# Kernel optimization log

Hardware: AMD Instinct MI355X
Metric: run time of the kernel (lower is better)

Reference implementation:

```python
import jax, jax.numpy as jnp
import numpy as np

NUM_USERS = 100000
NUM_ITEMS = 50000
N_NODES = NUM_USERS + NUM_ITEMS
EMB = 64          # emb_dim == layers[0]
NNZ = 2_400_000   # ~16 avg degree normalized-Laplacian nonzeros
BATCH = 16384


def spmm(rows, cols, vals, x, n):
    # sparse (COO) Laplacian @ dense features: out[r] += v * x[c]
    return jax.ops.segment_sum(vals[:, None] * x[cols], rows, num_segments=n)


def setup_inputs() -> dict:
    key = jax.random.key(0)
    ks = jax.random.split(key, 20)
    userIdx = jax.random.randint(ks[0], (BATCH,), 0, NUM_USERS)
    itemIdx = jax.random.randint(ks[1], (BATCH,), 0, NUM_ITEMS)
    lap_rows = jax.random.randint(ks[2], (NNZ,), 0, N_NODES, dtype=jnp.int32)
    lap_cols = jax.random.randint(ks[3], (NNZ,), 0, N_NODES, dtype=jnp.int32)
    # normalized Laplacian values ~ 1/sqrt(deg_i*deg_j), small positive
    lap_vals = jax.random.uniform(ks[4], (NNZ,), dtype=jnp.float32) * 0.05
    uEmb = jax.random.normal(ks[5], (NUM_USERS, EMB), dtype=jnp.float32) * 0.1
    iEmb = jax.random.normal(ks[6], (NUM_ITEMS, EMB), dtype=jnp.float32) * 0.1
    s = 1.0 / np.sqrt(EMB)
    gW0 = jax.random.normal(ks[7], (EMB, EMB), dtype=jnp.float32) * s
    gb0 = jnp.zeros((EMB,), jnp.float32)
    gW1 = jax.random.normal(ks[8], (EMB, EMB), dtype=jnp.float32) * s
    gb1 = jnp.zeros((EMB,), jnp.float32)
    D_CAT = EMB * 3 * 2  # 384
    W1 = jax.random.normal(ks[9], (D_CAT, 64), dtype=jnp.float32) / np.sqrt(D_CAT)
    b1 = jnp.zeros((64,), jnp.float32)
    W2 = jax.random.normal(ks[10], (64, 32), dtype=jnp.float32) / 8.0
    b2 = jnp.zeros((32,), jnp.float32)
    W3 = jax.random.normal(ks[11], (32, 1), dtype=jnp.float32) / np.sqrt(32.0)
    b3 = jnp.zeros((1,), jnp.float32)
    return {"userIdx": userIdx, "itemIdx": itemIdx,
            "lap_rows": lap_rows, "lap_cols": lap_cols, "lap_vals": lap_vals,
            "uEmb": uEmb, "iEmb": iEmb,
            "gW0": gW0, "gb0": gb0, "gW1": gW1, "gb1": gb1,
            "W1": W1, "b1": b1, "W2": W2, "b2": b2, "W3": W3, "b3": b3}


def reference(userIdx, itemIdx, lap_rows, lap_cols, lap_vals,
              uEmb, iEmb, gW0, gb0, gW1, gb1, W1, b1, W2, b2, W3, b3):
    features = jnp.concatenate([uEmb, iEmb], axis=0)  # [N, EMB]
    final = features
    for W, b in ((gW0, gb0), (gW1, gb1)):
        # (Laplacian + selfLoop I) @ features, then linear + ReLU
        h = spmm(lap_rows, lap_cols, lap_vals, features, N_NODES) + features
        features = jax.nn.relu(h @ W + b)
        final = jnp.concatenate([final, features], axis=1)
    u = final[userIdx]                     # [B, 192]
    it = final[itemIdx + NUM_USERS]        # [B, 192]
    e = jnp.concatenate([u, it], axis=1)   # [B, 384]
    e = jax.nn.relu(e @ W1 + b1)
    e = e @ W2 + b2
    e = e @ W3 + b3
    return e.ravel()
```

## Files before the change

kernel.cpp:

```cpp
#include <hip/hip_runtime.h>
#include <hip/hip_bf16.h>

#define NUM_USERS 100000
#define NUM_ITEMS 50000
#define N_NODES   150000
#define EMB       64
#define NNZ       2400000
#define BATCH     16384
#define D_CAT     384
#define BSHIFT    8
#define NBUCK     ((N_NODES + 255) >> 8)
#define EPB       8192

__device__ __forceinline__ unsigned short f2bf(float f) {
    unsigned u = __float_as_uint(f);
    unsigned r = u + 0x7fffu + ((u >> 16) & 1u);
    return (unsigned short)(r >> 16);
}
__device__ __forceinline__ float bflo(unsigned u) { return __uint_as_float(u << 16); }
__device__ __forceinline__ float bfhi(unsigned u) { return __uint_as_float(u & 0xffff0000u); }

__global__ __launch_bounds__(1024) void bucket_hist(const int* __restrict__ rows,
                                                    int* __restrict__ bcnt, int nnz) {
    __shared__ int h[NBUCK];
    int tid = threadIdx.x;
    for (int i = tid; i < NBUCK; i += 1024) h[i] = 0;
    __syncthreads();
    for (int i = blockIdx.x * 1024 + tid; i < nnz; i += gridDim.x * 1024)
        atomicAdd(&h[rows[i] >> BSHIFT], 1);
    __syncthreads();
    for (int i = tid; i < NBUCK; i += 1024) {
        int c = h[i];
        if (c) atomicAdd(&bcnt[i], c);
    }
}

__global__ __launch_bounds__(1024) void bucket_scan(const int* __restrict__ bcnt,
                                                    int* __restrict__ boffs,
                                                    int* __restrict__ gtails, int nnz) {
    __shared__ int s[1024];
    int t = threadIdx.x;
    int x = (t < NBUCK) ? bcnt[t] : 0;
    s[t] = x;
    __syncthreads();
#pragma unroll
    for (int off = 1; off < 1024; off <<= 1) {
        int v = (t >= off) ? s[t - off] : 0;
        __syncthreads();
        s[t] += v;
        __syncthreads();
    }
    if (t < NBUCK) {
        int e = s[t] - x;
        boffs[t] = e;
        gtails[t] = e;
    }
    if (t == 0) boffs[NBUCK] = nnz;
}

__global__ __launch_bounds__(1024) void coarse_multisplit(const int* __restrict__ rows,
                                                          const int* __restrict__ cols,
                                                          const float* __restrict__ vals,
                                                          int* __restrict__ gtails,
                                                          int2* __restrict__ pv, int nnz) {
    __shared__ int hcnt[NBUCK];
    int tid = threadIdx.x;
    int e0 = blockIdx.x * EPB;
    int e1 = e0 + EPB < nnz ? e0 + EPB : nnz;

    for (int i = tid; i < NBUCK; i += 1024) hcnt[i] = 0;
    __syncthreads();
    for (int i = e0 + tid; i < e1; i += 1024)
        atomicAdd(&hcnt[rows[i] >> BSHIFT], 1);
    __syncthreads();
    for (int i = tid; i < NBUCK; i += 1024) {
        int c = hcnt[i];
        if (c) hcnt[i] = atomicAdd(&gtails[i], c);
    }
    __syncthreads();
    for (int i = e0 + tid; i < e1; i += 1024) {
        int r = rows[i];
        int pos = atomicAdd(&hcnt[r >> BSHIFT], 1);
        pv[pos] = make_int2(((r & 255) << 18) | cols[i], __float_as_int(vals[i]));
    }
}

__global__ __launch_bounds__(1024) void fine_scatter(const int* __restrict__ boffs,
                                                     const int2* __restrict__ pv,
                                                     int2* __restrict__ packed,
                                                     int* __restrict__ row_ptr, int nnz) {
    __shared__ int rcnt[256];
    __shared__ int loff[256];
    int b = blockIdx.x;
    int tid = threadIdx.x;
    int lo = boffs[b], hi = boffs[b + 1];
    int r0 = b << BSHIFT;
    int nr = N_NODES - r0; if (nr > 256) nr = 256;

    if (tid < 256) rcnt[tid] = 0;
    __syncthreads();
    for (int i = lo + tid; i < hi; i += 1024)
        atomicAdd(&rcnt[pv[i].x >> 18], 1);
    __syncthreads();
    if (tid < 256) loff[tid] = rcnt[tid];
    __syncthreads();
#pragma unroll
    for (int off = 1; off < 256; off <<= 1) {
        int v = (tid < 256 && tid >= off) ? loff[tid - off] : 0;
        __syncthreads();
        if (tid < 256) loff[tid] += v;
        __syncthreads();
    }
    if (tid < 256) {
        int e = lo + loff[tid] - rcnt[tid];
        loff[tid] = e;
        if (tid < nr) row_ptr[r0 + tid] = e;
    }
    if (b == 0 && tid == 0) row_ptr[N_NODES] = nnz;
    __syncthreads();
    for (int i = lo + tid; i < hi; i += 1024) {
        int2 e = pv[i];
        int rl = e.x >> 18;
        int pos = atomicAdd(&loff[rl], 1);
        packed[pos] = make_int2(e.x & 0x3FFFF, e.y);
    }
}

__global__ __launch_bounds__(256) void gemm_table_f32(const float* __restrict__ uE,
                                                      const float* __restrict__ iE,
                                                      const float* __restrict__ W,
                                                      unsigned short* __restrict__ Zh,
                                                      int n_rows) {
    __shared__ float Wl[64 * 64];
    __shared__ float Xf[64 * 64];
    int tid = threadIdx.x;
    int lane = tid & 63;
    int wave = tid >> 6;
    int r0 = blockIdx.x * 64;
    int last = n_rows - 1;

    for (int i = tid; i < 64 * 64; i += 256) Wl[i] = W[i];
    for (int i = tid; i < 64 * 16; i += 256) {
        int row = i >> 4, q = i & 15;
        int r = r0 + row; r = r > last ? last : r;
        const float4* src = (r < NUM_USERS)
            ? (const float4*)(uE + (size_t)r * 64)
            : (const float4*)(iE + (size_t)(r - NUM_USERS) * 64);
        ((float4*)Xf)[i] = src[q];
    }
    __syncthreads();

    int rbase = wave * 16;
    float acc[16];
#pragma unroll
    for (int i = 0; i < 16; ++i) acc[i] = 0.f;

#pragma unroll 1
    for (int kc = 0; kc < 16; ++kc) {
        float w0 = Wl[(kc * 4 + 0) * 64 + lane];
        float w1 = Wl[(kc * 4 + 1) * 64 + lane];
        float w2 = Wl[(kc * 4 + 2) * 64 + lane];
        float w3 = Wl[(kc * 4 + 3) * 64 + lane];
#pragma unroll
        for (int i = 0; i < 16; ++i) {
            float4 q = ((const float4*)Xf)[(rbase + i) * 16 + kc];
            acc[i] = fmaf(q.x, w0, acc[i]);
            acc[i] = fmaf(q.y, w1, acc[i]);
            acc[i] = fmaf(q.z, w2, acc[i]);
            acc[i] = fmaf(q.w, w3, acc[i]);
        }
    }
#pragma unroll
    for (int i = 0; i < 16; ++i) {
        int r = r0 + rbase + i;
        if (r < n_rows) Zh[(size_t)r * 64 + lane] = f2bf(acc[i]);
    }
}

__global__ __launch_bounds__(256) void gemm_table_bf16(const unsigned* __restrict__ Xh,
                                                       const float* __restrict__ W,
                                                       unsigned short* __restrict__ Zh,
                                                       int n_rows) {
    __shared__ float Wl[64 * 64];
    __shared__ uint4 Xl4[64 * 8];
    int tid = threadIdx.x;
    int lane = tid & 63;
    int wave = tid >> 6;
    int r0 = blockIdx.x * 64;
    int nr = n_rows - r0; if (nr > 64) nr = 64;

    for (int i = tid; i < 64 * 64; i += 256) Wl[i] = W[i];
    const uint4* Xg4 = (const uint4*)(Xh + (size_t)r0 * 32);
    for (int i = tid; i < nr * 8; i += 256) Xl4[i] = Xg4[i];
    __syncthreads();

    const unsigned* Xl = (const unsigned*)Xl4;
    int rbase = wave * 16;
    float acc[16];
#pragma unroll
    for (int i = 0; i < 16; ++i) acc[i] = 0.f;

#pragma unroll 1
    for (int kc = 0; kc < 8; ++kc) {
        float w0 = Wl[(kc * 8 + 0) * 64 + lane];
        float w1 = Wl[(kc * 8 + 1) * 64 + lane];
        float w2 = Wl[(kc * 8 + 2) * 64 + lane];
        float w3 = Wl[(kc * 8 + 3) * 64 + lane];
        float w4 = Wl[(kc * 8 + 4) * 64 + lane];
        float w5 = Wl[(kc * 8 + 5) * 64 + lane];
        float w6 = Wl[(kc * 8 + 6) * 64 + lane];
        float w7 = Wl[(kc * 8 + 7) * 64 + lane];
#pragma unroll
        for (int i = 0; i < 16; ++i) {
            uint4 q = *(const uint4*)&Xl[(rbase + i) * 32 + kc * 4];
            acc[i] = fmaf(bflo(q.x), w0, acc[i]);
            acc[i] = fmaf(bfhi(q.x), w1, acc[i]);
            acc[i] = fmaf(bflo(q.y), w2, acc[i]);
            acc[i] = fmaf(bfhi(q.y), w3, acc[i]);
            acc[i] = fmaf(bflo(q.z), w4, acc[i]);
            acc[i] = fmaf(bfhi(q.z), w5, acc[i]);
            acc[i] = fmaf(bflo(q.w), w6, acc[i]);
            acc[i] = fmaf(bfhi(q.w), w7, acc[i]);
        }
    }
#pragma unroll
    for (int i = 0; i < 16; ++i) {
        int r = r0 + rbase + i;
        if (r < n_rows) Zh[(size_t)r * 64 + lane] = f2bf(acc[i]);
    }
}

__global__ __launch_bounds__(256) void spmm_bias_relu(const int* __restrict__ row_ptr,
                                                      const int2* __restrict__ packed,
                                                      const uint2* __restrict__ zh2,
                                                      const float* __restrict__ bias,
                                                      uint2* __restrict__ outh2,
                                                      int n_rows) {
    int tid = threadIdx.x;
    int lane = tid & 63;
    int wave = tid >> 6;
    int q = lane >> 4;
    int k = lane & 15;
    int r = blockIdx.x * 4 + wave;
    if (r >= n_rows) return;

    uint2 su = zh2[(size_t)r * 16 + k];
    float4 acc;
    acc.x = q ? 0.f : bflo(su.x);
    acc.y = q ? 0.f : bfhi(su.x);
    acc.z = q ? 0.f : bflo(su.y);
    acc.w = q ? 0.f : bfhi(su.y);

    int e = row_ptr[r] + q;
    int end = row_ptr[r + 1];
    for (; e + 13 < end; e += 16) {
        int2 p0 = packed[e + 0];
        int2 p1 = packed[e + 4];
        int2 p2 = packed[e + 8];
        int2 p3 = packed[e + 12];
        uint2 z0 = zh2[(size_t)p0.x * 16 + k];
        uint2 z1 = zh2[(size_t)p1.x * 16 + k];
        uint2 z2 = zh2[(size_t)p2.x * 16 + k];
        uint2 z3 = zh2[(size_t)p3.x * 16 + k];
        float v0 = __int_as_float(p0.y), v1 = __int_as_float(p1.y);
        float v2 = __int_as_float(p2.y), v3 = __int_as_float(p3.y);
        acc.x = fmaf(v0, bflo(z0.x), acc.x); acc.y = fmaf(v0, bfhi(z0.x), acc.y);
        acc.z = fmaf(v0, bflo(z0.y), acc.z); acc.w = fmaf(v0, bfhi(z0.y), acc.w);
        acc.x = fmaf(v1, bflo(z1.x), acc.x); acc.y = fmaf(v1, bfhi(z1.x), acc.y);
        acc.z = fmaf(v1, bflo(z1.y), acc.z); acc.w = fmaf(v1, bfhi(z1.y), acc.w);
        acc.x = fmaf(v2, bflo(z2.x), acc.x); acc.y = fmaf(v2, bfhi(z2.x), acc.y);
        acc.z = fmaf(v2, bflo(z2.y), acc.z); acc.w = fmaf(v2, bfhi(z2.y), acc.w);
        acc.x = fmaf(v3, bflo(z3.x), acc.x); acc.y = fmaf(v3, bfhi(z3.x), acc.y);
        acc.z = fmaf(v3, bflo(z3.y), acc.z); acc.w = fmaf(v3, bfhi(z3.y), acc.w);
    }
    for (; e < end; e += 4) {
        int2 p = packed[e];
        uint2 z = zh2[(size_t)p.x * 16 + k];
        float v = __int_as_float(p.y);
        acc.x = fmaf(v, bflo(z.x), acc.x); acc.y = fmaf(v, bfhi(z.x), acc.y);
        acc.z = fmaf(v, bflo(z.y), acc.z); acc.w = fmaf(v, bfhi(z.y), acc.w);
    }

    acc.x += __shfl_xor(acc.x, 16, 64);
    acc.y += __shfl_xor(acc.y, 16, 64);
    acc.z += __shfl_xor(acc.z, 16, 64);
    acc.w += __shfl_xor(acc.w, 16, 64);
    acc.x += __shfl_xor(acc.x, 32, 64);
    acc.y += __shfl_xor(acc.y, 32, 64);
    acc.z += __shfl_xor(acc.z, 32, 64);
    acc.w += __shfl_xor(acc.w, 32, 64);
    if (q == 0) {
        float4 bv = ((const float4*)bias)[k];
        float a = fmaxf(acc.x + bv.x, 0.f);
        float b = fmaxf(acc.y + bv.y, 0.f);
        float c = fmaxf(acc.z + bv.z, 0.f);
        float d = fmaxf(acc.w + bv.w, 0.f);
        outh2[(size_t)r * 16 + k] = make_uint2(
            ((unsigned)f2bf(b) << 16) | (unsigned)f2bf(a),
            ((unsigned)f2bf(d) << 16) | (unsigned)f2bf(c));
    }
}

__global__ __launch_bounds__(384) void gather_e(const int* __restrict__ userIdx,
                                                const int* __restrict__ itemIdx,
                                                const float* __restrict__ uEmb,
                                                const float* __restrict__ iEmb,
                                                const unsigned short* __restrict__ feat1h,
                                                const unsigned short* __restrict__ feat2h,
                                                unsigned short* __restrict__ E) {
    int b = blockIdx.x;
    int j = threadIdx.x;
    int half = j >= 192;
    int jj = half ? (j - 192) : j;
    int seg = jj >> 6;
    int k = jj & 63;
    unsigned short v;
    if (half == 0) {
        int u = userIdx[b];
        if (seg == 0)      v = f2bf(uEmb[(size_t)u * 64 + k]);
        else if (seg == 1) v = feat1h[(size_t)u * 64 + k];
        else               v = feat2h[(size_t)u * 64 + k];
    } else {
        int it = itemIdx[b];
        if (seg == 0)      v = f2bf(iEmb[(size_t)it * 64 + k]);
        else if (seg == 1) v = feat1h[(size_t)(it + NUM_USERS) * 64 + k];
        else               v = feat2h[(size_t)(it + NUM_USERS) * 64 + k];
    }
    E[(size_t)b * D_CAT + j] = v;
}

__global__ __launch_bounds__(256) void gemm384_bf16_relu(const unsigned short* __restrict__ E,
                                                         const float* __restrict__ W,
                                                         const float* __restrict__ bia,
                                                         float* __restrict__ H1,
                                                         int n_rows) {
    __shared__ float Wl[128 * 64];
    __shared__ uint4 El[64 * 16];
    int tid = threadIdx.x;
    int lane = tid & 63;
    int wave = tid >> 6;
    int r0 = blockIdx.x * 64;
    int rbase = wave * 16;
    int last = n_rows - 1;

    float acc[16];
    float bv = bia[lane];
#pragma unroll
    for (int i = 0; i < 16; ++i) acc[i] = bv;

    for (int k0 = 0; k0 < D_CAT; k0 += 128) {
        if (k0) __syncthreads();
        for (int i = tid; i < 128 * 64; i += 256) Wl[i] = W[k0 * 64 + i];
        for (int i = tid; i < 64 * 16; i += 256) {
            int row = i >> 4, q = i & 15;
            int r = r0 + row; r = r > last ? last : r;
            El[i] = *(const uint4*)(E + (size_t)r * D_CAT + k0 + q * 8);
        }
        __syncthreads();
#pragma unroll 1
        for (int k = 0; k < 128; k += 8) {
            float w0 = Wl[(k + 0) * 64 + lane];
            float w1 = Wl[(k + 1) * 64 + lane];
            float w2 = Wl[(k + 2) * 64 + lane];
            float w3 = Wl[(k + 3) * 64 + lane];
            float w4 = Wl[(k + 4) * 64 + lane];
            float w5 = Wl[(k + 5) * 64 + lane];
            float w6 = Wl[(k + 6) * 64 + lane];
            float w7 = Wl[(k + 7) * 64 + lane];
#pragma unroll
            for (int i = 0; i < 16; ++i) {
                uint4 q = El[(rbase + i) * 16 + (k >> 3)];
                acc[i] = fmaf(bflo(q.x), w0, acc[i]);
                acc[i] = fmaf(bfhi(q.x), w1, acc[i]);
                acc[i] = fmaf(bflo(q.y), w2, acc[i]);
                acc[i] = fmaf(bfhi(q.y), w3, acc[i]);
                acc[i] = fmaf(bflo(q.z), w4, acc[i]);
                acc[i] = fmaf(bfhi(q.z), w5, acc[i]);
                acc[i] = fmaf(bflo(q.w), w6, acc[i]);
                acc[i] = fmaf(bfhi(q.w), w7, acc[i]);
            }
        }
    }
#pragma unroll
    for (int i = 0; i < 16; ++i) {
        int r = r0 + rbase + i;
        if (r < n_rows) H1[(size_t)r * 64 + lane] = fmaxf(acc[i], 0.f);
    }
}

__global__ __launch_bounds__(256) void mlp23(const float* __restrict__ H1,
                                             const float* __restrict__ W2,
                                             const float* __restrict__ b2,
                                             const float* __restrict__ W3,
                                             const float* __restrict__ b3,
                                             float* __restrict__ out) {
    __shared__ float Wl[64 * 32];
    __shared__ float w3l[32];
    __shared__ float b2l[32];
    int tid = threadIdx.x;
    for (int i = tid; i < 64 * 32; i += 256) Wl[i] = W2[i];
    if (tid < 32) { w3l[tid] = W3[tid]; b2l[tid] = b2[tid]; }
    __syncthreads();

    int lane = tid & 63;
    int wave = tid >> 6;
    int half = lane >> 5;
    int k = lane & 31;
    int gpair = blockIdx.x * 4 + wave;
    int npairs = gridDim.x * 4;
    float b3v = b3[0];
    for (int p = gpair; p * 2 < BATCH; p += npairs) {
        int r = p * 2 + half;
        float acc = b2l[k];
#pragma unroll
        for (int j = 0; j < 64; ++j)
            acc += H1[(size_t)r * 64 + j] * Wl[j * 32 + k];
        acc = acc * w3l[k];
#pragma unroll
        for (int off = 16; off; off >>= 1)
            acc += __shfl_xor(acc, off, 64);
        if (k == 0) out[r] = acc + b3v;
    }
}

extern "C" void kernel_launch(void* const* d_in, const int* in_sizes, int n_in,
                              void* d_out, int out_size, void* d_ws, size_t ws_size,
                              hipStream_t stream) {
    const int*   userIdx = (const int*)  d_in[0];
    const int*   itemIdx = (const int*)  d_in[1];
    const int*   lap_rows= (const int*)  d_in[2];
    const int*   lap_cols= (const int*)  d_in[3];
    const float* lap_vals= (const float*)d_in[4];
    const float* uEmb    = (const float*)d_in[5];
    const float* iEmb    = (const float*)d_in[6];
    const float* gW0     = (const float*)d_in[7];
    const float* gb0     = (const float*)d_in[8];
    const float* gW1     = (const float*)d_in[9];
    const float* gb1     = (const float*)d_in[10];
    const float* W1      = (const float*)d_in[11];
    const float* b1      = (const float*)d_in[12];
    const float* W2      = (const float*)d_in[13];
    const float* b2      = (const float*)d_in[14];
    const float* W3      = (const float*)d_in[15];
    const float* b3      = (const float*)d_in[16];
    float* out = (float*)d_out;

    const size_t NF = (size_t)N_NODES * EMB;
    char* w = (char*)d_ws;
    unsigned short* bufA = (unsigned short*)w;
    unsigned short* bufB = bufA + NF;
    char*  region3 = (char*)(bufB + NF);
    int2*  pv      = (int2*)region3;
    unsigned short* Zh = (unsigned short*)region3;
    unsigned short* E  = (unsigned short*)region3;
    float* H1 = (float*)(E + (size_t)BATCH * D_CAT);
    int2*  packed  = (int2*)(region3 + NF * sizeof(float));
    int*   row_ptr = (int*)(packed + NNZ);
    int*   boffs   = row_ptr + (N_NODES + 1);
    int*   gtails  = boffs + (NBUCK + 1);
    int*   bcnt    = gtails + NBUCK;

    const int ms_grid   = (NNZ + EPB - 1) / EPB;
    const int spmm_grid = (N_NODES + 3) / 4;
    const int gemm_grid = (N_NODES + 63) / 64;

    hipMemsetAsync(bcnt, 0, NBUCK * sizeof(int), stream);
    bucket_hist<<<128, 1024, 0, stream>>>(lap_rows, bcnt, NNZ);
    bucket_scan<<<1, 1024, 0, stream>>>(bcnt, boffs, gtails, NNZ);
    coarse_multisplit<<<ms_grid, 1024, 0, stream>>>(lap_rows, lap_cols, lap_vals,
                                                    gtails, pv, NNZ);
    fine_scatter<<<NBUCK, 1024, 0, stream>>>(boffs, pv, packed, row_ptr, NNZ);

    gemm_table_f32<<<gemm_grid, 256, 0, stream>>>(uEmb, iEmb, gW0, Zh, N_NODES);
    spmm_bias_relu<<<spmm_grid, 256, 0, stream>>>(row_ptr, packed, (const uint2*)Zh,
                                                  gb0, (uint2*)bufA, N_NODES);

    gemm_table_bf16<<<gemm_grid, 256, 0, stream>>>((const unsigned*)bufA, gW1, Zh, N_NODES);
    spmm_bias_relu<<<spmm_grid, 256, 0, stream>>>(row_ptr, packed, (const uint2*)Zh,
                                                  gb1, (uint2*)bufB, N_NODES);

    gather_e<<<BATCH, 384, 0, stream>>>(userIdx, itemIdx, uEmb, iEmb, bufA, bufB, E);

    gemm384_bf16_relu<<<(BATCH + 63) / 64, 256, 0, stream>>>(E, W1, b1, H1, BATCH);
    mlp23<<<512, 256, 0, stream>>>(H1, W2, b2, W3, b3, out);
}
```

Measured before the change: 517.4 us.

## Fuse embedding gather, first MLP layer and output head into one kernel

Replaces the separate gather_e, gemm384 and mlp23 kernels with a single kernel per 64-row batch tile. The tile gathers user/item rows straight into shared memory, runs the 384x64 layer, keeps the hidden activations in shared memory and finishes the 64->32->1 head locally. This removes two launches and the global round trips through the E and H1 buffers. In exchange it uses more shared memory per block (about 66 KB), which may lower occupancy, and the head stage runs on only 256 blocks.

New measurement: 492.5 us. 1.05x faster.

```diff
diff --git a/kernel.cpp b/kernel.cpp
--- a/kernel.cpp
+++ b/kernel.cpp
@@ -301,62 +301,70 @@
     }
 }
 
-__global__ __launch_bounds__(384) void gather_e(const int* __restrict__ userIdx,
-                                                const int* __restrict__ itemIdx,
-                                                const float* __restrict__ uEmb,
-                                                const float* __restrict__ iEmb,
-                                                const unsigned short* __restrict__ feat1h,
-                                                const unsigned short* __restrict__ feat2h,
-                                                unsigned short* __restrict__ E) {
-    int b = blockIdx.x;
-    int j = threadIdx.x;
-    int half = j >= 192;
-    int jj = half ? (j - 192) : j;
-    int seg = jj >> 6;
-    int k = jj & 63;
-    unsigned short v;
-    if (half == 0) {
-        int u = userIdx[b];
-        if (seg == 0)      v = f2bf(uEmb[(size_t)u * 64 + k]);
-        else if (seg == 1) v = feat1h[(size_t)u * 64 + k];
-        else               v = feat2h[(size_t)u * 64 + k];
-    } else {
-        int it = itemIdx[b];
-        if (seg == 0)      v = f2bf(iEmb[(size_t)it * 64 + k]);
-        else if (seg == 1) v = feat1h[(size_t)(it + NUM_USERS) * 64 + k];
-        else               v = feat2h[(size_t)(it + NUM_USERS) * 64 + k];
-    }
-    E[(size_t)b * D_CAT + j] = v;
-}
-
-__global__ __launch_bounds__(256) void gemm384_bf16_relu(const unsigned short* __restrict__ E,
-                                                         const float* __restrict__ W,
-                                                         const float* __restrict__ bia,
-                                                         float* __restrict__ H1,
-                                                         int n_rows) {
-    __shared__ float Wl[128 * 64];
-    __shared__ uint4 El[64 * 16];
+__global__ __launch_bounds__(256) void fused_mlp(
+        const int* __restrict__ userIdx, const int* __restrict__ itemIdx,
+        const float* __restrict__ uEmb, const float* __restrict__ iEmb,
+        const unsigned short* __restrict__ feat1h,
+        const unsigned short* __restrict__ feat2h,
+        const float* __restrict__ W1, const float* __restrict__ b1,
+        const float* __restrict__ W2, const float* __restrict__ b2,
+        const float* __restrict__ W3, const float* __restrict__ b3,
+        float* __restrict__ out) {
+    __shared__ float    Wl[128 * 64];
+    __shared__ unsigned El[64 * 64];
+    __shared__ float    Ht[64 * 64];
+    __shared__ float    W2l[64 * 32];
+    __shared__ float    w3l[32];
+    __shared__ float    b2l[32];
+    __shared__ int      uidx[64], iidx[64];
     int tid = threadIdx.x;
     int lane = tid & 63;
     int wave = tid >> 6;
     int r0 = blockIdx.x * 64;
     int rbase = wave * 16;
-    int last = n_rows - 1;
+
+    if (tid < 64) uidx[tid] = userIdx[r0 + tid];
+    else if (tid < 128) iidx[tid - 64] = itemIdx[r0 + tid - 64];
+    if (tid < 32) { w3l[tid] = W3[tid]; b2l[tid] = b2[tid]; }
+    for (int i = tid; i < 64 * 32; i += 256) W2l[i] = W2[i];
 
     float acc[16];
-    float bv = bia[lane];
+    float bv = b1[lane];
 #pragma unroll
     for (int i = 0; i < 16; ++i) acc[i] = bv;
 
-    for (int k0 = 0; k0 < D_CAT; k0 += 128) {
-        if (k0) __syncthreads();
-        for (int i = tid; i < 128 * 64; i += 256) Wl[i] = W[k0 * 64 + i];
-        for (int i = tid; i < 64 * 16; i += 256) {
-            int row = i >> 4, q = i & 15;
-            int r = r0 + row; r = r > last ? last : r;
-            El[i] = *(const uint4*)(E + (size_t)r * D_CAT + k0 + q * 8);
+#pragma unroll 1
+    for (int c = 0; c < 3; ++c) {
+        __syncthreads();
+        for (int i = tid; i < 128 * 64; i += 256) Wl[i] = W1[c * 128 * 64 + i];
+        for (int t = tid; t < 1024; t += 256) {
+            int row = t >> 4;
+            int seg = (t >> 3) & 1;
+            int q   = t & 7;
+            int gseg = c * 2 + seg;
+            uint4 val;
+            if (gseg == 0 || gseg == 3) {
+                const float* p = (gseg == 0)
+                    ? uEmb + (size_t)uidx[row] * 64 + q * 8
+                    : iEmb + (size_t)iidx[row] * 64 + q * 8;
+                float4 a = *(const float4*)p;
+                float4 b = *(const float4*)(p + 4);
+                val.x = ((unsigned)f2bf(a.y) << 16) | f2bf(a.x);
+                val.y = ((unsigned)f2bf(a.w) << 16) | f2bf(a.z);
+                val.z = ((unsigned)f2bf(b.y) << 16) | f2bf(b.x);
+                val.w = ((unsigned)f2bf(b.w) << 16) | f2bf(b.z);
+            } else {
+                const unsigned short* src;
+                if (gseg == 1)      src = feat1h + (size_t)uidx[row] * 64;
+                else if (gseg == 2) src = feat2h + (size_t)uidx[row] * 64;
+                else if (gseg == 4) src = feat1h + (size_t)(iidx[row] + NUM_USERS) * 64;
+                else                src = feat2h + (size_t)(iidx[row] + NUM_USERS) * 64;
+                val = *(const uint4*)(src + q * 8);
+            }
+            *(uint4*)&El[row * 64 + seg * 32 + q * 4] = val;
         }
         __syncthreads();
+        const uint4* El4 = (const uint4*)El;
 #pragma unroll 1
         for (int k = 0; k < 128; k += 8) {
             float w0 = Wl[(k + 0) * 64 + lane];
@@ -369,7 +377,7 @@
             float w7 = Wl[(k + 7) * 64 + lane];
 #pragma unroll
             for (int i = 0; i < 16; ++i) {
-                uint4 q = El[(rbase + i) * 16 + (k >> 3)];
+                uint4 q = El4[(rbase + i) * 16 + (k >> 3)];
                 acc[i] = fmaf(bflo(q.x), w0, acc[i]);
                 acc[i] = fmaf(bfhi(q.x), w1, acc[i]);
                 acc[i] = fmaf(bflo(q.y), w2, acc[i]);
@@ -381,45 +389,26 @@
             }
         }
     }
-#pragma unroll
-    for (int i = 0; i < 16; ++i) {
-        int r = r0 + rbase + i;
-        if (r < n_rows) H1[(size_t)r * 64 + lane] = fmaxf(acc[i], 0.f);
-    }
-}
-
-__global__ __launch_bounds__(256) void mlp23(const float* __restrict__ H1,
-                                             const float* __restrict__ W2,
-                                             const float* __restrict__ b2,
-                                             const float* __restrict__ W3,
-                                             const float* __restrict__ b3,
-                                             float* __restrict__ out) {
-    __shared__ float Wl[64 * 32];
-    __shared__ float w3l[32];
-    __shared__ float b2l[32];
-    int tid = threadIdx.x;
-    for (int i = tid; i < 64 * 32; i += 256) Wl[i] = W2[i];
-    if (tid < 32) { w3l[tid] = W3[tid]; b2l[tid] = b2[tid]; }
-    __syncthreads();
-
-    int lane = tid & 63;
-    int wave = tid >> 6;
+
+#pragma unroll
+    for (int i = 0; i < 16; ++i) Ht[(rbase + i) * 64 + lane] = fmaxf(acc[i], 0.f);
+    __syncthreads();
+
     int half = lane >> 5;
     int k = lane & 31;
-    int gpair = blockIdx.x * 4 + wave;
-    int npairs = gridDim.x * 4;
     float b3v = b3[0];
-    for (int p = gpair; p * 2 < BATCH; p += npairs) {
-        int r = p * 2 + half;
-        float acc = b2l[k];
+#pragma unroll 1
+    for (int p = 0; p < 8; ++p) {
+        int row = rbase + p * 2 + half;
+        float z = b2l[k];
 #pragma unroll
         for (int j = 0; j < 64; ++j)
-            acc += H1[(size_t)r * 64 + j] * Wl[j * 32 + k];
-        acc = acc * w3l[k];
+            z = fmaf(Ht[row * 64 + j], W2l[j * 32 + k], z);
+        z *= w3l[k];
 #pragma unroll
         for (int off = 16; off; off >>= 1)
-            acc += __shfl_xor(acc, off, 64);
-        if (k == 0) out[r] = acc + b3v;
+            z += __shfl_xor(z, off, 64);
+        if (k == 0) out[r0 + row] = z + b3v;
     }
 }
 
@@ -452,8 +441,6 @@
     char*  region3 = (char*)(bufB + NF);
     int2*  pv      = (int2*)region3;
     unsigned short* Zh = (unsigned short*)region3;
-    unsigned short* E  = (unsigned short*)region3;
-    float* H1 = (float*)(E + (size_t)BATCH * D_CAT);
     int2*  packed  = (int2*)(region3 + NF * sizeof(float));
     int*   row_ptr = (int*)(packed + NNZ);
     int*   boffs   = row_ptr + (N_NODES + 1);
@@ -479,8 +466,6 @@
     spmm_bias_relu<<<spmm_grid, 256, 0, stream>>>(row_ptr, packed, (const uint2*)Zh,
                                                   gb1, (uint2*)bufB, N_NODES);
 
-    gather_e<<<BATCH, 384, 0, stream>>>(userIdx, itemIdx, uEmb, iEmb, bufA, bufB, E);
-
-    gemm384_bf16_relu<<<(BATCH + 63) / 64, 256, 0, stream>>>(E, W1, b1, H1, BATCH);
-    mlp23<<<512, 256, 0, stream>>>(H1, W2, b2, W3, b3, out);
-}
+    fused_mlp<<<BATCH / 64, 256, 0, stream>>>(userIdx, itemIdx, uEmb, iEmb,
+                                              bufA, bufB, W1, b1, W2, b2, W3, b3, out);
+}
```
